# Performance work log

Measured on AMD Instinct MI355X. Metric: run time of the kernel, lower is better.

The kernel has to match this reference:

```python
import jax, jax.numpy as jnp
import numpy as np

T, B, I, H, LBL = 200, 1024, 128, 128, 4


def setup_inputs() -> dict:
    key = jax.random.key(0)
    ks = jax.random.split(key, 14)
    si = 1.0 / np.sqrt(I)
    sh = 1.0 / np.sqrt(H)
    inputs = jax.random.normal(ks[0], (T, B, I), jnp.float32)
    lengths = jnp.maximum(jax.random.randint(ks[1], (B,), 1, T + 1), LBL).astype(jnp.int32)
    return {
        "inputs": inputs,
        "lengths": lengths,
        "Wih_g": jax.random.normal(ks[2], (3 * H, I), jnp.float32) * si,
        "Whh_g": jax.random.normal(ks[3], (3 * H, H), jnp.float32) * sh,
        "bih_g": jax.random.normal(ks[4], (3 * H,), jnp.float32) * sh,
        "bhh_g": jax.random.normal(ks[5], (3 * H,), jnp.float32) * sh,
        "Wih_l": jax.random.normal(ks[6], (3 * H, I), jnp.float32) * si,
        "Whh_l": jax.random.normal(ks[7], (3 * H, H), jnp.float32) * sh,
        "bih_l": jax.random.normal(ks[8], (3 * H,), jnp.float32) * sh,
        "bhh_l": jax.random.normal(ks[9], (3 * H,), jnp.float32) * sh,
        "A1": jax.random.normal(ks[10], (H, H), jnp.float32) * sh,
        "A2": jax.random.normal(ks[11], (H, H), jnp.float32) * sh,
        "v1": jax.random.normal(ks[12], (1, H), jnp.float32) * sh,
        "label_len": LBL,
    }


def gru(x, Wih, Whh, bih, bhh):
    # x: [T, B, I] time-major. PyTorch GRU cell semantics.
    Bq, Hq = x.shape[1], Whh.shape[1]
    gi_all = jnp.einsum('tbi,gi->tbg', x, Wih) + bih  # precompute input projections [T,B,3H]
    def step(h, gi):
        gh = h @ Whh.T + bhh
        ir, iz, inn = jnp.split(gi, 3, axis=-1)
        hr, hz, hn = jnp.split(gh, 3, axis=-1)
        r = jax.nn.sigmoid(ir + hr)
        z = jax.nn.sigmoid(iz + hz)
        n = jnp.tanh(inn + r * hn)
        h = (1.0 - z) * n + z * h
        return h, h
    h0 = jnp.zeros((Bq, Hq), x.dtype)
    _, hs = jax.lax.scan(step, h0, gi_all)
    return hs  # [T, B, H]


def reference(inputs, lengths, Wih_g, Whh_g, bih_g, bhh_g,
              Wih_l, Whh_l, bih_l, bhh_l, A1, A2, v1, label_len):
    h_g = gru(inputs, Wih_g, Whh_g, bih_g, bhh_g)  # [T,B,H]
    h_l = gru(inputs, Wih_l, Whh_l, bih_l, bhh_l)  # [T,B,H]
    # attention score per step s: v1(sigmoid(A1 h_l + A2 h_g)), query-independent
    pre = jax.nn.sigmoid(jnp.einsum('tbh,gh->tbg', h_l, A1) +
                         jnp.einsum('tbh,gh->tbg', h_g, A2))
    scores = jnp.einsum('tbg,og->tbo', pre, v1)  # [T,B,1]
    # per-t output = cumsum_{s<=t}(score*h_l) + h_g[t]
    out = jnp.cumsum(scores * h_l, axis=0) + h_g  # [T,B,H]
    out_b = jnp.transpose(out, (1, 0, 2))  # [B,T,H]
    # gather last label_len timesteps of each sequence: h[b,k] = out[L_b-label_len+k, b]
    idx = lengths[:, None].astype(jnp.int32) - label_len + jnp.arange(label_len, dtype=jnp.int32)[None, :]
    idx = jnp.clip(idx, 0, out_b.shape[1] - 1)  # [B, label_len]
    h = jnp.take_along_axis(out_b, idx[:, :, None], axis=1)  # [B, label_len, H]
    return h
```

## Files before the change

kernel.cpp:

```cpp
#include <hip/hip_runtime.h>
#include <stdint.h>


typedef __attribute__((ext_vector_type(8))) short short8;
typedef __attribute__((ext_vector_type(4))) float float4v;

#define LDS_BARRIER() asm volatile("s_waitcnt lgkmcnt(0)\n\ts_barrier" ::: "memory")

__device__ inline float bf2f(unsigned short u){
  union { unsigned int i; float f; } v; v.i = ((unsigned int)u) << 16; return v.f;
}
__device__ inline unsigned short f2bf(float f){
  union { float f; unsigned int i; } v; v.f = f;
  unsigned int x = v.i;
  return (unsigned short)((x + 0x7fffu + ((x >> 16) & 1u)) >> 16);
}
__device__ inline unsigned int pack2(float a, float b){
  return (unsigned int)f2bf(a) | ((unsigned int)f2bf(b) << 16);
}
__device__ inline float sigm(float x){ return __builtin_amdgcn_rcpf(1.0f + __expf(-x)); }

__global__ void k_prep(unsigned short* hl_slot, unsigned short* hg_slot, float* cum,
                       const float* A1, const float* A2, unsigned short* a12)
{
  int i = blockIdx.x * blockDim.x + threadIdx.x;
  hl_slot[i] = 0;
  hg_slot[i] = 0;
  cum[i] = 0.0f;
  if (i < 32768) {
    a12[i] = f2bf((i < 16384) ? A1[i] : A2[i - 16384]);
  }
}

__global__ __launch_bounds__(512, 2) void k_scan(
    const float* __restrict__ x,
    const float* __restrict__ Wih_g, const float* __restrict__ Whh_g,
    const float* __restrict__ bih_g, const float* __restrict__ bhh_g,
    const float* __restrict__ Wih_l, const float* __restrict__ Whh_l,
    const float* __restrict__ bih_l, const float* __restrict__ bhh_l,
    unsigned short* __restrict__ hl_seq, unsigned short* __restrict__ hg_seq,
    int tc, int t0)
{
  __shared__ __align__(16) unsigned short hbuf[2][16][136];
  __shared__ __align__(16) unsigned short xbuf[2][16][136];
  int tid = threadIdx.x;
  int w = tid >> 6, L = tid & 63, l15 = L & 15, q = L >> 4;
  int gru = blockIdx.x & 1;
  int b0 = (blockIdx.x >> 1) * 16;
  const float* Wih = gru ? Wih_l : Wih_g;
  const float* Whh = gru ? Whh_l : Whh_g;
  const float* bih = gru ? bih_l : bih_g;
  const float* bhh = gru ? bhh_l : bhh_g;
  unsigned short* myseq = gru ? hl_seq : hg_seq;

  int col = w * 16 + l15;

  short8 Wi[3][4], Wh[3][4];
  #pragma unroll
  for (int G = 0; G < 3; G++) {
    int row = G * 128 + col;
    #pragma unroll
    for (int kf = 0; kf < 4; kf++) {
      const float4* p0 = (const float4*)(Wih + (size_t)row * 128 + kf * 32 + q * 8);
      const float4* p1 = (const float4*)(Whh + (size_t)row * 128 + kf * 32 + q * 8);
      float4 a0 = p0[0], a1 = p0[1], b0f = p1[0], b1f = p1[1];
      short8 si, sh;
      si[0]=(short)f2bf(a0.x); si[1]=(short)f2bf(a0.y); si[2]=(short)f2bf(a0.z); si[3]=(short)f2bf(a0.w);
      si[4]=(short)f2bf(a1.x); si[5]=(short)f2bf(a1.y); si[6]=(short)f2bf(a1.z); si[7]=(short)f2bf(a1.w);
      sh[0]=(short)f2bf(b0f.x); sh[1]=(short)f2bf(b0f.y); sh[2]=(short)f2bf(b0f.z); sh[3]=(short)f2bf(b0f.w);
      sh[4]=(short)f2bf(b1f.x); sh[5]=(short)f2bf(b1f.y); sh[6]=(short)f2bf(b1f.z); sh[7]=(short)f2bf(b1f.w);
      Wi[G][kf] = si; Wh[G][kf] = sh;
    }
  }
  float br  = bih[col]       + bhh[col];
  float bz  = bih[128 + col] + bhh[128 + col];
  float bin = bih[256 + col];
  float bnh = bhh[256 + col];

  float hold[4];
  #pragma unroll
  for (int r = 0; r < 4; r++) {
    int m = q * 4 + r;
    unsigned short u = myseq[((size_t)(tc - 1) * 1024 + b0 + m) * 128 + col];
    hold[r] = bf2f(u);
    hbuf[0][m][col] = u;
  }
  int xrow = tid >> 5, xc4 = (tid & 31) * 4;
  {
    float4 x0 = ((const float4*)(x + ((size_t)t0 * 1024 + b0) * 128))[tid];
    *(uint2*)&xbuf[0][xrow][xc4] = make_uint2(pack2(x0.x, x0.y), pack2(x0.z, x0.w));
  }
  int tn = t0 + (tc > 1 ? 1 : 0);
  float4 xr = ((const float4*)(x + ((size_t)tn * 1024 + b0) * 128))[tid];
  __syncthreads();

  unsigned short* opq = myseq + ((size_t)(b0 + q * 4)) * 128 + col;

  auto step = [&](int s, int pin, int pout) {
    short8 Ax[4], Ah[4];
    #pragma unroll
    for (int kf = 0; kf < 4; kf++) Ax[kf] = *(const short8*)&xbuf[pin][l15][kf * 32 + q * 8];
    #pragma unroll
    for (int kf = 0; kf < 4; kf++) Ah[kf] = *(const short8*)&hbuf[pin][l15][kf * 32 + q * 8];

    *(uint2*)&xbuf[pout][xrow][xc4] = make_uint2(pack2(xr.x, xr.y), pack2(xr.z, xr.w));
    {
      int t2 = t0 + (s + 2 < tc ? s + 2 : tc - 1);
      xr = ((const float4*)(x + ((size_t)t2 * 1024 + b0) * 128))[tid];
    }

    float4v rx = (float4v){0.f,0.f,0.f,0.f}, zx = rx, nx = rx;
    float4v rh = rx, zh = rx, nh = rx;
    #pragma unroll
    for (int kf = 0; kf < 4; kf++) rx = __builtin_amdgcn_mfma_f32_16x16x32_bf16(Ax[kf], Wi[0][kf], rx, 0,0,0);
    #pragma unroll
    for (int kf = 0; kf < 4; kf++) zx = __builtin_amdgcn_mfma_f32_16x16x32_bf16(Ax[kf], Wi[1][kf], zx, 0,0,0);
    #pragma unroll
    for (int kf = 0; kf < 4; kf++) nx = __builtin_amdgcn_mfma_f32_16x16x32_bf16(Ax[kf], Wi[2][kf], nx, 0,0,0);
    #pragma unroll
    for (int kf = 0; kf < 4; kf++) rh = __builtin_amdgcn_mfma_f32_16x16x32_bf16(Ah[kf], Wh[0][kf], rh, 0,0,0);
    #pragma unroll
    for (int kf = 0; kf < 4; kf++) zh = __builtin_amdgcn_mfma_f32_16x16x32_bf16(Ah[kf], Wh[1][kf], zh, 0,0,0);
    #pragma unroll
    for (int kf = 0; kf < 4; kf++) nh = __builtin_amdgcn_mfma_f32_16x16x32_bf16(Ah[kf], Wh[2][kf], nh, 0,0,0);

    float cr[4], cz[4], cn[4];
    #pragma unroll
    for (int r = 0; r < 4; r++) { cr[r] = rx[r] + br; cz[r] = zx[r] + bz; cn[r] = nx[r] + bin; }

    #pragma unroll
    for (int r = 0; r < 4; r++) {
      float er = __expf(-(rh[r] + cr[r]));
      float ez = __expf(-(zh[r] + cz[r]));
      float pr = 1.0f + er, pz = 1.0f + ez;
      float inv = __builtin_amdgcn_rcpf(pr * pz);
      float rr = pz * inv;
      float zz = pr * inv;
      float y  = cn[r] + rr * (nh[r] + bnh);
      float em = __expf(-2.0f * y);
      float nn = 2.0f * __builtin_amdgcn_rcpf(1.0f + em) - 1.0f;
      float hn = nn + zz * (hold[r] - nn);
      hold[r] = hn;
      unsigned short hu = f2bf(hn);
      hbuf[pout][q * 4 + r][col] = hu;
      opq[r * 128] = hu;
    }
    opq += 131072;
    LDS_BARRIER();
  };

  int s = 0;
  for (; s + 1 < tc; s += 2) { step(s, 0, 1); step(s + 1, 1, 0); }
  if (s < tc) step(s, 0, 1);
}

__global__ __launch_bounds__(512) void k_score(const unsigned short* __restrict__ hl_seq,
                                               const unsigned short* __restrict__ hg_seq,
                                               const unsigned short* __restrict__ a12,
                                               const float* __restrict__ v1,
                                               float* __restrict__ score, int tc)
{
  __shared__ __align__(16) unsigned short M1[128][136];
  __shared__ __align__(16) unsigned short M2[128][136];
  int tid = threadIdx.x;
  int w = tid >> 6, L = tid & 63;
  int l15 = L & 15, q = L >> 4;
  int s = blockIdx.x;
  int bhalf = blockIdx.y * 512;

  #pragma unroll
  for (int it = 0; it < 4; it++) {
    int f8 = it * 512 + tid;
    *(short8*)&M1[f8 >> 4][(f8 & 15) * 8] = *(const short8*)(a12 + (size_t)f8 * 8);
    *(short8*)&M2[f8 >> 4][(f8 & 15) * 8] = *(const short8*)(a12 + 16384 + (size_t)f8 * 8);
  }
  __syncthreads();

  float v1v[8];
  #pragma unroll
  for (int nt = 0; nt < 8; nt++) v1v[nt] = v1[nt * 16 + l15];

  short8 Fl[4], Fg[4], Pl[4], Pg[4];
  {
    size_t base = ((size_t)s * 1024 + bhalf + (size_t)w * 16 + l15) * 128;
    #pragma unroll
    for (int kf = 0; kf < 4; kf++) {
      Fl[kf] = *(const short8*)(hl_seq + base + kf * 32 + q * 8);
      Fg[kf] = *(const short8*)(hg_seq + base + kf * 32 + q * 8);
    }
  }
  #pragma unroll
  for (int it = 0; it < 4; it++) {
    int b0 = bhalf + (it * 8 + w) * 16;
    if (it + 1 < 4) {
      size_t base = ((size_t)s * 1024 + bhalf + (size_t)((it + 1) * 8 + w) * 16 + l15) * 128;
      #pragma unroll
      for (int kf = 0; kf < 4; kf++) {
        Pl[kf] = *(const short8*)(hl_seq + base + kf * 32 + q * 8);
        Pg[kf] = *(const short8*)(hg_seq + base + kf * 32 + q * 8);
      }
    }
    float4v acc[8];
    #pragma unroll
    for (int nt = 0; nt < 8; nt++) {
      float4v a = (float4v){0.f, 0.f, 0.f, 0.f};
      #pragma unroll
      for (int kf = 0; kf < 4; kf++)
        a = __builtin_amdgcn_mfma_f32_16x16x32_bf16(
            Fl[kf], *(const short8*)&M1[nt * 16 + l15][kf * 32 + q * 8], a, 0, 0, 0);
      #pragma unroll
      for (int kf = 0; kf < 4; kf++)
        a = __builtin_amdgcn_mfma_f32_16x16x32_bf16(
            Fg[kf], *(const short8*)&M2[nt * 16 + l15][kf * 32 + q * 8], a, 0, 0, 0);
      acc[nt] = a;
    }
    float p4[4];
    #pragma unroll
    for (int r = 0; r < 4; r++) {
      float sum = 0.f;
      #pragma unroll
      for (int nt = 0; nt < 8; nt++) sum += v1v[nt] * sigm(acc[nt][r]);
      sum += __shfl_xor(sum, 1, 16);
      sum += __shfl_xor(sum, 2, 16);
      sum += __shfl_xor(sum, 4, 16);
      sum += __shfl_xor(sum, 8, 16);
      p4[r] = sum;
    }
    if (l15 == 0) {
      #pragma unroll
      for (int r = 0; r < 4; r++)
        score[(size_t)(b0 + q * 4 + r) * tc + s] = p4[r];
    }
    #pragma unroll
    for (int kf = 0; kf < 4; kf++) { Fl[kf] = Pl[kf]; Fg[kf] = Pg[kf]; }
  }
}

__global__ __launch_bounds__(256) void k_cum(const float* __restrict__ score,
                                             const unsigned short* __restrict__ hl_seq,
                                             const unsigned short* __restrict__ hg_seq,
                                             const int* __restrict__ lengths,
                                             float* __restrict__ cum,
                                             float* __restrict__ out, int tc, int t0)
{
  __shared__ __align__(16) unsigned short hlL[100 * 256];
  __shared__ float scL[2][100];
  int tid = threadIdx.x;
  int b2 = tid >> 7, j = tid & 127;
  int b0 = blockIdx.x * 2;
  int b = b0 + b2;
  int base = b2 * 128 + j;

  float c = cum[(size_t)b * 128 + j];
  int cap0 = lengths[b] - 4;

  float hgv[4];
  #pragma unroll
  for (int d = 0; d < 4; d++) {
    int sl = cap0 + d - t0;
    hgv[d] = (sl >= 0 && sl < tc) ? bf2f(hg_seq[((size_t)sl * 1024 + b) * 128 + j]) : 0.f;
  }

  for (int seg = 0; seg < tc; seg += 100) {
    int len = (tc - seg < 100) ? (tc - seg) : 100;
    __syncthreads();
    for (int f8 = tid; f8 < len * 32; f8 += 256) {
      int sl = f8 >> 5, r8 = f8 & 31;
      *(short8*)&hlL[(size_t)f8 * 8] =
          *(const short8*)(hl_seq + ((size_t)(seg + sl) * 1024 + b0) * 128 + r8 * 8);
    }
    for (int i = tid; i < 2 * len; i += 256) {
      int bb = (i >= len) ? 1 : 0;
      int sl = i - bb * len;
      scL[bb][sl] = score[(size_t)(b0 + bb) * tc + seg + sl];
    }
    __syncthreads();

    int sl = 0;
    for (; sl + 5 <= len; sl += 5) {
      float h[5], sc[5];
      #pragma unroll
      for (int k = 0; k < 5; k++) {
        h[k] = bf2f(hlL[(size_t)(sl + k) * 256 + base]);
        sc[k] = scL[b2][sl + k];
      }
      #pragma unroll
      for (int k = 0; k < 5; k++) {
        c += sc[k] * h[k];
        int d = (t0 + seg + sl + k) - cap0;
        if ((unsigned)d < 4u)
          out[((size_t)b * 4 + d) * 128 + j] = c + hgv[d];
      }
    }
    for (; sl < len; sl++) {
      c += scL[b2][sl] * bf2f(hlL[(size_t)sl * 256 + base]);
      int d = (t0 + seg + sl) - cap0;
      if ((unsigned)d < 4u)
        out[((size_t)b * 4 + d) * 128 + j] = c + hgv[d];
    }
  }
  cum[(size_t)b * 128 + j] = c;
}

extern "C" void kernel_launch(void* const* d_in, const int* in_sizes, int n_in,
                              void* d_out, int out_size, void* d_ws, size_t ws_size,
                              hipStream_t stream)
{
  const float* x     = (const float*)d_in[0];
  const int* lengths = (const int*)d_in[1];
  const float* Wih_g = (const float*)d_in[2];
  const float* Whh_g = (const float*)d_in[3];
  const float* bih_g = (const float*)d_in[4];
  const float* bhh_g = (const float*)d_in[5];
  const float* Wih_l = (const float*)d_in[6];
  const float* Whh_l = (const float*)d_in[7];
  const float* bih_l = (const float*)d_in[8];
  const float* bhh_l = (const float*)d_in[9];
  const float* A1    = (const float*)d_in[10];
  const float* A2    = (const float*)d_in[11];
  const float* v1    = (const float*)d_in[12];
  float* out = (float*)d_out;

  const size_t fixed = 65536 + 524288;
  const int cands[7] = {200, 100, 50, 10, 4, 2, 1};
  int tc = 0;
  for (int i = 0; i < 7; i++) {
    int T = cands[i];
    size_t need = 2 * (size_t)T * 1024 * 128 * 2
                + (size_t)T * 1024 * 4
                + fixed;
    if (need <= ws_size) { tc = T; break; }
  }
  if (!tc) return;

  char* wsb = (char*)d_ws;
  size_t o = 0;
  unsigned short* a12 = (unsigned short*)(wsb + o); o += 65536;
  float* cum   = (float*)(wsb + o); o += 524288;
  unsigned short* hl  = (unsigned short*)(wsb + o); o += (size_t)tc * 1024 * 128 * 2;
  unsigned short* hg  = (unsigned short*)(wsb + o); o += (size_t)tc * 1024 * 128 * 2;
  float* score = (float*)(wsb + o);

  unsigned short* hl_slot = hl + (size_t)(tc - 1) * 1024 * 128;
  unsigned short* hg_slot = hg + (size_t)(tc - 1) * 1024 * 128;

  k_prep<<<512, 256, 0, stream>>>(hl_slot, hg_slot, cum, A1, A2, a12);
  int nch = 200 / tc;
  for (int c = 0; c < nch; c++) {
    k_scan<<<128, 512, 0, stream>>>(x, Wih_g, Whh_g, bih_g, bhh_g,
                                    Wih_l, Whh_l, bih_l, bhh_l, hl, hg, tc, c * tc);
    k_score<<<dim3(tc, 2), 512, 0, stream>>>(hl, hg, a12, v1, score, tc);
    k_cum<<<512, 256, 0, stream>>>(score, hl, hg, lengths, cum, out, tc, c * tc);
  }
}
```

Before: 402.1 us.

## Pre-cast inputs to bf16 and load x fragments directly into registers

A new kernel converts the whole fp32 input sequence to bf16 once into workspace. The scan kernel then loads MFMA A-fragments for x straight from global memory into a double-buffered register set, removing the x LDS staging buffer and its per-step convert/store. The hidden-state LDS buffer gets a fragment-friendly layout written as packed 32-bit pairs via a lane shuffle. In exchange it adds an extra full-tensor pass and workspace, plus uncoalesced 16-byte global loads on the serial critical path.

```diff
diff --git a/kernel.cpp b/kernel.cpp
--- a/kernel.cpp
+++ b/kernel.cpp
@@ -32,8 +32,19 @@
   }
 }
 
+__global__ void k_xcast(const float* __restrict__ x, unsigned short* __restrict__ xb)
+{
+  size_t i = (size_t)blockIdx.x * blockDim.x + threadIdx.x;
+  const float4* xf = (const float4*)x;
+  float4 a = xf[2 * i], b = xf[2 * i + 1];
+  short8 o;
+  o[0]=(short)f2bf(a.x); o[1]=(short)f2bf(a.y); o[2]=(short)f2bf(a.z); o[3]=(short)f2bf(a.w);
+  o[4]=(short)f2bf(b.x); o[5]=(short)f2bf(b.y); o[6]=(short)f2bf(b.z); o[7]=(short)f2bf(b.w);
+  *(short8*)(xb + i * 8) = o;
+}
+
 __global__ __launch_bounds__(512, 2) void k_scan(
-    const float* __restrict__ x,
+    const unsigned short* __restrict__ xb,
     const float* __restrict__ Wih_g, const float* __restrict__ Whh_g,
     const float* __restrict__ bih_g, const float* __restrict__ bhh_g,
     const float* __restrict__ Wih_l, const float* __restrict__ Whh_l,
@@ -41,8 +52,7 @@
     unsigned short* __restrict__ hl_seq, unsigned short* __restrict__ hg_seq,
     int tc, int t0)
 {
-  __shared__ __align__(16) unsigned short hbuf[2][16][136];
-  __shared__ __align__(16) unsigned short xbuf[2][16][136];
+  __shared__ __align__(16) unsigned short hb[2][2048];
   int tid = threadIdx.x;
   int w = tid >> 6, L = tid & 63, l15 = L & 15, q = L >> 4;
   int gru = blockIdx.x & 1;
@@ -83,40 +93,49 @@
     int m = q * 4 + r;
     unsigned short u = myseq[((size_t)(tc - 1) * 1024 + b0 + m) * 128 + col];
     hold[r] = bf2f(u);
-    hbuf[0][m][col] = u;
-  }
-  int xrow = tid >> 5, xc4 = (tid & 31) * 4;
+    hb[0][(col >> 3) * 128 + m * 8 + (col & 7)] = u;
+  }
+
+  short8 x2[2][4];
+  const unsigned short* xlane = xb + ((size_t)b0 + l15) * 128 + q * 8;
   {
-    float4 x0 = ((const float4*)(x + ((size_t)t0 * 1024 + b0) * 128))[tid];
-    *(uint2*)&xbuf[0][xrow][xc4] = make_uint2(pack2(x0.x, x0.y), pack2(x0.z, x0.w));
-  }
-  int tn = t0 + (tc > 1 ? 1 : 0);
-  float4 xr = ((const float4*)(x + ((size_t)tn * 1024 + b0) * 128))[tid];
+    const unsigned short* px = xlane + (size_t)t0 * 131072;
+    #pragma unroll
+    for (int kf = 0; kf < 4; kf++) x2[0][kf] = *(const short8*)(px + kf * 32);
+    int t1 = t0 + (tc > 1 ? 1 : 0);
+    const unsigned short* py = xlane + (size_t)t1 * 131072;
+    #pragma unroll
+    for (int kf = 0; kf < 4; kf++) x2[1][kf] = *(const short8*)(py + kf * 32);
+  }
   __syncthreads();
 
   unsigned short* opq = myseq + ((size_t)(b0 + q * 4)) * 128 + col;
+  unsigned int* hbw = (unsigned int*)&hb[0][0];
+  int wdw = (2 * w + (l15 >> 3)) * 64 + ((l15 & 6) >> 1);
+  bool wlane = (L & 1) == 0;
 
   auto step = [&](int s, int pin, int pout) {
-    short8 Ax[4], Ah[4];
-    #pragma unroll
-    for (int kf = 0; kf < 4; kf++) Ax[kf] = *(const short8*)&xbuf[pin][l15][kf * 32 + q * 8];
-    #pragma unroll
-    for (int kf = 0; kf < 4; kf++) Ah[kf] = *(const short8*)&hbuf[pin][l15][kf * 32 + q * 8];
-
-    *(uint2*)&xbuf[pout][xrow][xc4] = make_uint2(pack2(xr.x, xr.y), pack2(xr.z, xr.w));
+    short8 Ah[4];
+    #pragma unroll
+    for (int kf = 0; kf < 4; kf++)
+      Ah[kf] = *(const short8*)&hb[pin][(kf * 4 + q) * 128 + l15 * 8];
+
+    float4v rx = (float4v){0.f,0.f,0.f,0.f}, zx = rx, nx = rx;
+    #pragma unroll
+    for (int kf = 0; kf < 4; kf++) rx = __builtin_amdgcn_mfma_f32_16x16x32_bf16(x2[pin][kf], Wi[0][kf], rx, 0,0,0);
+    #pragma unroll
+    for (int kf = 0; kf < 4; kf++) zx = __builtin_amdgcn_mfma_f32_16x16x32_bf16(x2[pin][kf], Wi[1][kf], zx, 0,0,0);
+    #pragma unroll
+    for (int kf = 0; kf < 4; kf++) nx = __builtin_amdgcn_mfma_f32_16x16x32_bf16(x2[pin][kf], Wi[2][kf], nx, 0,0,0);
+
     {
       int t2 = t0 + (s + 2 < tc ? s + 2 : tc - 1);
-      xr = ((const float4*)(x + ((size_t)t2 * 1024 + b0) * 128))[tid];
-    }
-
-    float4v rx = (float4v){0.f,0.f,0.f,0.f}, zx = rx, nx = rx;
-    float4v rh = rx, zh = rx, nh = rx;
-    #pragma unroll
-    for (int kf = 0; kf < 4; kf++) rx = __builtin_amdgcn_mfma_f32_16x16x32_bf16(Ax[kf], Wi[0][kf], rx, 0,0,0);
-    #pragma unroll
-    for (int kf = 0; kf < 4; kf++) zx = __builtin_amdgcn_mfma_f32_16x16x32_bf16(Ax[kf], Wi[1][kf], zx, 0,0,0);
-    #pragma unroll
-    for (int kf = 0; kf < 4; kf++) nx = __builtin_amdgcn_mfma_f32_16x16x32_bf16(Ax[kf], Wi[2][kf], nx, 0,0,0);
+      const unsigned short* px = xlane + (size_t)t2 * 131072;
+      #pragma unroll
+      for (int kf = 0; kf < 4; kf++) x2[pin][kf] = *(const short8*)(px + kf * 32);
+    }
+
+    float4v rh = (float4v){0.f,0.f,0.f,0.f}, zh = rh, nh = rh;
     #pragma unroll
     for (int kf = 0; kf < 4; kf++) rh = __builtin_amdgcn_mfma_f32_16x16x32_bf16(Ah[kf], Wh[0][kf], rh, 0,0,0);
     #pragma unroll
@@ -128,6 +147,7 @@
     #pragma unroll
     for (int r = 0; r < 4; r++) { cr[r] = rx[r] + br; cz[r] = zx[r] + bz; cn[r] = nx[r] + bin; }
 
+    unsigned int* hbo = hbw + pout * 1024 + wdw;
     #pragma unroll
     for (int r = 0; r < 4; r++) {
       float er = __expf(-(rh[r] + cr[r]));
@@ -142,8 +162,10 @@
       float hn = nn + zz * (hold[r] - nn);
       hold[r] = hn;
       unsigned short hu = f2bf(hn);
-      hbuf[pout][q * 4 + r][col] = hu;
       opq[r * 128] = hu;
+      unsigned int hv = (unsigned int)hu;
+      unsigned int ov = (unsigned int)__shfl_xor((int)hv, 1);
+      if (wlane) hbo[(4 * q + r) * 4] = hv | (ov << 16);
     }
     opq += 131072;
     LDS_BARRIER();
@@ -321,10 +343,11 @@
   const float* v1    = (const float*)d_in[12];
   float* out = (float*)d_out;
 
-  const size_t fixed = 65536 + 524288;
-  const int cands[7] = {200, 100, 50, 10, 4, 2, 1};
+  const size_t XB = (size_t)200 * 1024 * 128 * 2;
+  const size_t fixed = 65536 + 524288 + XB;
+  const int cands[8] = {200, 100, 50, 25, 10, 5, 2, 1};
   int tc = 0;
-  for (int i = 0; i < 7; i++) {
+  for (int i = 0; i < 8; i++) {
     int T = cands[i];
     size_t need = 2 * (size_t)T * 1024 * 128 * 2
                 + (size_t)T * 1024 * 4
@@ -337,6 +360,7 @@
   size_t o = 0;
   unsigned short* a12 = (unsigned short*)(wsb + o); o += 65536;
   float* cum   = (float*)(wsb + o); o += 524288;
+  unsigned short* xb = (unsigned short*)(wsb + o); o += XB;
   unsigned short* hl  = (unsigned short*)(wsb + o); o += (size_t)tc * 1024 * 128 * 2;
   unsigned short* hg  = (unsigned short*)(wsb + o); o += (size_t)tc * 1024 * 128 * 2;
   float* score = (float*)(wsb + o);
@@ -345,9 +369,10 @@
   unsigned short* hg_slot = hg + (size_t)(tc - 1) * 1024 * 128;
 
   k_prep<<<512, 256, 0, stream>>>(hl_slot, hg_slot, cum, A1, A2, a12);
+  k_xcast<<<12800, 256, 0, stream>>>(x, xb);
   int nch = 200 / tc;
   for (int c = 0; c < nch; c++) {
-    k_scan<<<128, 512, 0, stream>>>(x, Wih_g, Whh_g, bih_g, bhh_g,
+    k_scan<<<128, 512, 0, stream>>>(xb, Wih_g, Whh_g, bih_g, bhh_g,
                                     Wih_l, Whh_l, bih_l, bhh_l, hl, hg, tc, c * tc);
     k_score<<<dim3(tc, 2), 512, 0, stream>>>(hl, hg, a12, v1, score, tc);
     k_cum<<<512, 256, 0, stream>>>(score, hl, hg, lengths, cum, out, tc, c * tc);
```

New measurement: 432.0 us. 1.07x slower.
